# Performance work log

Hardware: AMD Instinct MI355X
Metric: run time of the kernel (lower is better)

## Reference

```python
import jax, jax.numpy as jnp
import numpy as np

MARGIN = 1.0
ALFA = 0.1


def setup_inputs() -> dict:
    key = jax.random.key(0)
    k1, k2 = jax.random.split(key)
    N, D, T = 262144, 128, 262144
    embeddings = jax.random.normal(k1, (N, D), dtype=jnp.float32)
    triplets = jax.random.randint(k2, (T, 3), 0, N, dtype=jnp.int64)
    return {"embeddings": embeddings, "triplets": triplets}


def _corr_loss(embeddings):
    # torch_cov(rowvar=False): columns are variables -> D x D covariance
    N, D = embeddings.shape
    m = embeddings - jnp.mean(embeddings, axis=0, keepdims=True)  # [N, D]
    cov = jnp.einsum('ni,nj->ij', m, m) / (N - 1)                 # [D, D]
    V = jnp.diagonal(cov)                                          # variances
    corr2 = (cov / jnp.sqrt(V[:, None] * V[None, :])) ** 2
    # strict lower triangle, n*(n-1)/2 elements, then mean
    tril = jnp.tril(jnp.ones((D, D), dtype=corr2.dtype), k=-1)
    return jnp.sum(corr2 * tril) / (D * (D - 1) / 2)


def _triplet_loss(embeddings, triplets):
    pivot = embeddings[triplets[:, 0]]
    positives = embeddings[triplets[:, 1]]
    negatives = embeddings[triplets[:, 2]]
    ap = jnp.sum((pivot - positives) ** 2, axis=1)
    an = jnp.sum((pivot - negatives) ** 2, axis=1)
    return jnp.mean(jax.nn.relu(ap - an + MARGIN))


def reference(embeddings, triplets):
    corr_loss = _corr_loss(embeddings)
    triplet_loss = _triplet_loss(embeddings, triplets)
    return triplet_loss + ALFA * corr_loss
```

## Files before the change

kernel.cpp:

```cpp
#include <hip/hip_runtime.h>

#define D 128
#define MARGIN 1.0f
#define ALFA 0.1f
#define KC 64
#define GRAMB 512
#define RBLK 520
#define TB 2048
#define GB 512

#define WS_TSUM   0
#define WS_GRAM   256
#define WS_COLSUM (WS_GRAM + D * D)
#define WS_ZERO   (WS_COLSUM + D)
#define WS_PART   16896
#define PART_STRIDE (D * D + D)
#define WS_TAB_F  (WS_PART + GRAMB * PART_STRIDE)

typedef __attribute__((ext_vector_type(8)))  short bf16x8;
typedef __attribute__((ext_vector_type(8)))  unsigned short u16x8;
typedef __attribute__((ext_vector_type(16))) float f32x16;

__device__ __forceinline__ unsigned short f2bf(float f) {
    unsigned u = __float_as_uint(f);
    u += 0x7FFFu + ((u >> 16) & 1u);
    return (unsigned short)(u >> 16);
}
__device__ __forceinline__ float bf2f(unsigned short u) {
    return __uint_as_float((unsigned)u << 16);
}

__device__ __forceinline__ void lds_barrier() {
    asm volatile("s_waitcnt lgkmcnt(0)" ::: "memory");
    __builtin_amdgcn_s_barrier();
}

__global__ __launch_bounds__(512, 4) void gram_mfma_write(const float* __restrict__ emb,
                                                          int rowsPerBlock,
                                                          float* __restrict__ ws,
                                                          unsigned short* __restrict__ tab) {
    __shared__ __align__(16) char lds[2][128 * 128];
    __shared__ float csred[D];

    const int tid = threadIdx.x;
    const int l   = tid & 63;
    const int w   = tid >> 6;
    const int r0  = blockIdx.x * rowsPerBlock;

    const int rT = w & 3;
    const int c0 = (w >> 2) * 2;

    f32x16 acc0 = {};
    f32x16 acc1 = {};
    float cs[4] = {0.f, 0.f, 0.f, 0.f};
    const int d0 = (tid & 31) * 4;

    auto stage = [&](int cc, int b) {
#pragma unroll
        for (int j = 0; j < 2; ++j) {
            const int k = j * 32 + (tid >> 5) * 2;
            const int rowg = r0 + cc * KC + k;
            const float* base = emb + (size_t)rowg * D + d0;
            float4 a  = *(const float4*)base;
            float4 bv = *(const float4*)(base + D);
            ushort4 ua, ub;
            unsigned short* pa = (unsigned short*)&ua;
            unsigned short* pb = (unsigned short*)&ub;
#pragma unroll
            for (int i = 0; i < 4; ++i) {
                float av = ((const float*)&a)[i];
                float bb = ((const float*)&bv)[i];
                cs[i] += av + bb;
                unsigned short ha = f2bf(av), hb = f2bf(bb);
                pa[i] = ha; pb[i] = hb;
                unsigned slotp = (unsigned)(k >> 3) ^ (unsigned)((tid & 31) & 7);
                unsigned off = (unsigned)(d0 + i) * 128u + slotp * 16u + (unsigned)((k & 7) << 1);
                *(unsigned*)(&lds[b][off]) = (unsigned)ha | ((unsigned)hb << 16);
            }
            *(ushort4*)&tab[(size_t)rowg * D + d0]       = ua;
            *(ushort4*)&tab[(size_t)(rowg + 1) * D + d0] = ub;
        }
    };

    auto frag = [&](int t, int kb, int b) -> bf16x8 {
        const int d = t * 32 + (l & 31);
        const int k = kb + (l >> 5) * 8;
        unsigned slotp = (unsigned)(k >> 3) ^ ((unsigned)(d >> 2) & 7u);
        return *(const bf16x8*)(&lds[b][(unsigned)d * 128u + slotp * 16u]);
    };

    const int nChunks = rowsPerBlock / KC;
    stage(0, 0);
    for (int cc = 0; cc < nChunks; ++cc) {
        const int b = cc & 1;
        lds_barrier();
        if (cc + 1 < nChunks) stage(cc + 1, b ^ 1);
#pragma unroll
        for (int kb = 0; kb < KC; kb += 16) {
            bf16x8 fr = frag(rT,     kb, b);
            bf16x8 f0 = frag(c0,     kb, b);
            bf16x8 f1 = frag(c0 + 1, kb, b);
            acc0 = __builtin_amdgcn_mfma_f32_32x32x16_bf16(fr, f0, acc0, 0, 0, 0);
            acc1 = __builtin_amdgcn_mfma_f32_32x32x16_bf16(fr, f1, acc1, 0, 0, 0);
        }
    }
    __syncthreads();

    if (tid < D) csred[tid] = 0.f;
    __syncthreads();
#pragma unroll
    for (int i = 0; i < 4; ++i) atomicAdd(&csred[d0 + i], cs[i]);
    __syncthreads();

    float* gram   = ws + WS_PART + (size_t)blockIdx.x * PART_STRIDE;
    float* colsum = gram + D * D;

    if (tid < D) colsum[tid] = csred[tid];

    const int row_hi = (l >> 5) * 4;
    const int col    = l & 31;
#pragma unroll
    for (int reg = 0; reg < 16; ++reg) {
        const int row32 = (reg & 3) + 8 * (reg >> 2) + row_hi;
        const int gr    = (rT * 32 + row32) * D;
        gram[gr + c0 * 32 + col]       = acc0[reg];
        gram[gr + (c0 + 1) * 32 + col] = acc1[reg];
    }
}

__global__ __launch_bounds__(256) void triplet_red(const unsigned short* __restrict__ tab,
                                                   const int* __restrict__ trip,
                                                   int T,
                                                   float* __restrict__ ws) {
    __shared__ float red[16];
    const int tid = threadIdx.x;

    if (blockIdx.x < RBLK) {
        const int idx   = (blockIdx.x % 65) * 256 + tid;
        const int slice = blockIdx.x / 65;
        if (idx >= PART_STRIDE) return;
        const int per = GRAMB / 8;
        const float* part = ws + WS_PART;
        float s = 0.f;
        const int p0 = slice * per;
#pragma unroll 8
        for (int p = 0; p < per; ++p)
            s += part[(size_t)(p0 + p) * PART_STRIDE + idx];
        if (idx < D * D) atomicAdd(&ws[WS_GRAM + idx], s);
        else             atomicAdd(&ws[WS_COLSUM + (idx - D * D)], s);
        return;
    }

    const int li  = tid & 15;
    const int grp = ((blockIdx.x - RBLK) * 256 + tid) >> 4;
    const int NG  = (TB * 256) >> 4;

    float wsum = 0.f;

    for (int t0 = grp; t0 < T; t0 += 6 * NG) {
        u16x8 P[6], Q[6], R[6];
#pragma unroll
        for (int u = 0; u < 6; ++u) {
            const int t = t0 + u * NG;
            if (t < T) {
                const int i0 = trip[3 * t], i1 = trip[3 * t + 1], i2 = trip[3 * t + 2];
                P[u] = *(const u16x8*)&tab[(size_t)i0 * D + li * 8];
                Q[u] = *(const u16x8*)&tab[(size_t)i1 * D + li * 8];
                R[u] = *(const u16x8*)&tab[(size_t)i2 * D + li * 8];
            }
        }
#pragma unroll
        for (int u = 0; u < 6; ++u) {
            const int t = t0 + u * NG;
            if (t < T) {
                float s = 0.f;
#pragma unroll
                for (int e = 0; e < 8; ++e) {
                    float p  = bf2f(P[u][e]);
                    float dp = p - bf2f(Q[u][e]);
                    float dn = p - bf2f(R[u][e]);
                    s += dp * dp - dn * dn;
                }
#pragma unroll
                for (int off = 8; off; off >>= 1) s += __shfl_xor(s, off, 64);
                if (li == 0) wsum += fmaxf(s + MARGIN, 0.f);
            }
        }
    }

    if (li == 0) red[tid >> 4] = wsum;
    __syncthreads();
    if (tid == 0) {
        float b = 0.f;
#pragma unroll
        for (int i = 0; i < 16; ++i) b += red[i];
        atomicAdd(&ws[WS_TSUM], b);
    }
}

__global__ __launch_bounds__(256) void finalize_kernel(const float* __restrict__ ws,
                                                       float* __restrict__ out,
                                                       int N, int T) {
    const float* gram   = ws + WS_GRAM;
    const float* colsum = ws + WS_COLSUM;

    __shared__ float V[D];
    __shared__ float red[256];

    const int tid = threadIdx.x;
    const float invN   = 1.0f / (float)N;
    const float invNm1 = 1.0f / (float)(N - 1);

    if (tid < D) {
        float m = colsum[tid] * invN;
        V[tid] = (gram[tid * D + tid] - (float)N * m * m) * invNm1;
    }
    __syncthreads();

    float local = 0.f;
    for (int idx = tid; idx < D * D; idx += 256) {
        int i = idx >> 7, j = idx & 127;
        if (j < i) {
            float mi  = colsum[i] * invN;
            float mj  = colsum[j] * invN;
            float cov = (gram[idx] - (float)N * mi * mj) * invNm1;
            local += cov * cov / (V[i] * V[j]);
        }
    }
    red[tid] = local;
    __syncthreads();
    for (int s = 128; s > 0; s >>= 1) {
        if (tid < s) red[tid] += red[tid + s];
        __syncthreads();
    }
    if (tid == 0) {
        float corr_mean = red[0] / ((float)D * (float)(D - 1) * 0.5f);
        out[0] = ws[WS_TSUM] / (float)T + ALFA * corr_mean;
    }
}

__device__ __forceinline__ float d2diff(float4 p, float4 q, float4 r) {
    float ax = p.x - q.x, ay = p.y - q.y, az = p.z - q.z, aw = p.w - q.w;
    float bx = p.x - r.x, by = p.y - r.y, bz = p.z - r.z, bw = p.w - r.w;
    return (ax * ax + ay * ay + az * az + aw * aw)
         - (bx * bx + by * by + bz * bz + bw * bw);
}

__global__ __launch_bounds__(512, 4) void fused_fallback(const float* __restrict__ emb,
                                                         const int* __restrict__ trip,
                                                         int rowsPerBlock, int T,
                                                         float* __restrict__ ws) {
    __shared__ __align__(16) char lds[2][128 * 128];
    __shared__ float csred[D];
    const int tid = threadIdx.x;

    if (blockIdx.x < GB) {
        const int l = tid & 63, w = tid >> 6, r0 = blockIdx.x * rowsPerBlock;
        const int rT = w & 3, c0 = (w >> 2) * 2;
        f32x16 acc0 = {}, acc1 = {};
        float cs[4] = {0.f, 0.f, 0.f, 0.f};
        const int d0 = (tid & 31) * 4;

        auto stage = [&](int cc, int b) {
#pragma unroll
            for (int j = 0; j < 2; ++j) {
                const int k = j * 32 + (tid >> 5) * 2;
                const float* base = emb + (size_t)(r0 + cc * 64 + k) * D + d0;
                float4 a = *(const float4*)base;
                float4 bv = *(const float4*)(base + D);
#pragma unroll
                for (int i = 0; i < 4; ++i) {
                    float av = ((const float*)&a)[i], bb = ((const float*)&bv)[i];
                    cs[i] += av + bb;
                    unsigned slotp = (unsigned)(k >> 3) ^ (unsigned)((tid & 31) & 7);
                    unsigned off = (unsigned)(d0 + i) * 128u + slotp * 16u + (unsigned)((k & 7) << 1);
                    *(unsigned*)(&lds[b][off]) = (unsigned)f2bf(av) | ((unsigned)f2bf(bb) << 16);
                }
            }
        };
        auto frag = [&](int t, int kb, int b) -> bf16x8 {
            const int d = t * 32 + (l & 31);
            const int k = kb + (l >> 5) * 8;
            unsigned slotp = (unsigned)(k >> 3) ^ ((unsigned)(d >> 2) & 7u);
            return *(const bf16x8*)(&lds[b][(unsigned)d * 128u + slotp * 16u]);
        };
        const int nChunks = rowsPerBlock / 64;
        stage(0, 0);
        for (int cc = 0; cc < nChunks; ++cc) {
            const int b = cc & 1;
            __syncthreads();
            if (cc + 1 < nChunks) stage(cc + 1, b ^ 1);
#pragma unroll
            for (int kb = 0; kb < 64; kb += 16) {
                bf16x8 fr = frag(rT, kb, b);
                bf16x8 f0 = frag(c0, kb, b);
                bf16x8 f1 = frag(c0 + 1, kb, b);
                acc0 = __builtin_amdgcn_mfma_f32_32x32x16_bf16(fr, f0, acc0, 0, 0, 0);
                acc1 = __builtin_amdgcn_mfma_f32_32x32x16_bf16(fr, f1, acc1, 0, 0, 0);
            }
        }
        __syncthreads();
        if (tid < D) csred[tid] = 0.f;
        __syncthreads();
#pragma unroll
        for (int i = 0; i < 4; ++i) atomicAdd(&csred[d0 + i], cs[i]);
        __syncthreads();
        if (tid < D) atomicAdd(&ws[WS_COLSUM + tid], csred[tid]);
        const int row_hi = (l >> 5) * 4, col = l & 31;
#pragma unroll
        for (int reg = 0; reg < 16; ++reg) {
            const int row32 = (reg & 3) + 8 * (reg >> 2) + row_hi;
            const int gr = (rT * 32 + row32) * D;
            atomicAdd(&ws[WS_GRAM + gr + c0 * 32 + col], acc0[reg]);
            atomicAdd(&ws[WS_GRAM + gr + (c0 + 1) * 32 + col], acc1[reg]);
        }
    } else {
        const int li = tid & 31, hwl = tid >> 5;
        const int hw = (blockIdx.x - GB) * 16 + hwl;
        const int NH = 1024 * 16;
        float wsum = 0.f;
        for (int t0 = hw; t0 < T; t0 += 4 * NH) {
            float4 P[4], Q[4], R[4];
#pragma unroll
            for (int k = 0; k < 4; ++k) {
                const int t = t0 + k * NH;
                if (t < T) {
                    const int i0 = trip[3 * t], i1 = trip[3 * t + 1], i2 = trip[3 * t + 2];
                    P[k] = ((const float4*)(emb + (size_t)i0 * D))[li];
                    Q[k] = ((const float4*)(emb + (size_t)i1 * D))[li];
                    R[k] = ((const float4*)(emb + (size_t)i2 * D))[li];
                }
            }
#pragma unroll
            for (int k = 0; k < 4; ++k) {
                const int t = t0 + k * NH;
                if (t < T) {
                    float s = d2diff(P[k], Q[k], R[k]);
#pragma unroll
                    for (int off = 16; off; off >>= 1) s += __shfl_xor(s, off, 64);
                    if (li == 0) wsum += fmaxf(s + MARGIN, 0.f);
                }
            }
        }
        if (li == 0) csred[hwl] = wsum;
        __syncthreads();
        if (tid == 0) {
            float b = 0.f;
#pragma unroll
            for (int i = 0; i < 16; ++i) b += csred[i];
            atomicAdd(&ws[WS_TSUM], b);
        }
    }
}

extern "C" void kernel_launch(void* const* d_in, const int* in_sizes, int n_in,
                              void* d_out, int out_size, void* d_ws, size_t ws_size,
                              hipStream_t stream) {
    const float* emb  = (const float*)d_in[0];
    const int*   trip = (const int*)d_in[1];
    float*       out  = (float*)d_out;
    float*       ws   = (float*)d_ws;

    const int N = in_sizes[0] / D;
    const int T = in_sizes[1] / 3;

    hipMemsetAsync(d_ws, 0, WS_ZERO * sizeof(float), stream);

    const size_t needB = (size_t)WS_TAB_F * 4 + (size_t)N * D * 2;

    if (ws_size >= needB) {
        unsigned short* tab = (unsigned short*)(ws + WS_TAB_F);
        gram_mfma_write<<<GRAMB, 512, 0, stream>>>(emb, N / GRAMB, ws, tab);
        triplet_red<<<RBLK + TB, 256, 0, stream>>>(tab, trip, T, ws);
    } else {
        fused_fallback<<<GB + 1024, 512, 0, stream>>>(emb, trip, N / GB, T, ws);
    }

    finalize_kernel<<<1, 256, 0, stream>>>(ws, out, N, T);
}
```

Measured before the change: 279.6 us.

## Split bf16 conversion into own kernel and co-schedule Gram MFMA with triplet gather

Separates the fp32-to-bf16 conversion and column sums into a streaming convert kernel. The Gram MFMA accumulation now reads the bf16 table and runs in the same launch as the triplet gather blocks, and the partial-Gram reduction moves to a separate kernel. The aim is to overlap the compute-bound Gram work with the latency-bound gather and to halve the partial-Gram count (256 instead of 512). The cost is an extra launch and an extra bf16 read of the table by the Gram blocks.

```diff
diff --git a/kernel.cpp b/kernel.cpp
--- a/kernel.cpp
+++ b/kernel.cpp
@@ -4,9 +4,9 @@
 #define MARGIN 1.0f
 #define ALFA 0.1f
 #define KC 64
-#define GRAMB 512
-#define RBLK 520
-#define TB 2048
+#define CVB 1024
+#define G2 256
+#define TB 1024
 #define GB 512
 
 #define WS_TSUM   0
@@ -14,8 +14,8 @@
 #define WS_COLSUM (WS_GRAM + D * D)
 #define WS_ZERO   (WS_COLSUM + D)
 #define WS_PART   16896
-#define PART_STRIDE (D * D + D)
-#define WS_TAB_F  (WS_PART + GRAMB * PART_STRIDE)
+#define PSTRIDE   (D * D)
+#define WS_TAB_F  (WS_PART + G2 * PSTRIDE)
 
 typedef __attribute__((ext_vector_type(8)))  short bf16x8;
 typedef __attribute__((ext_vector_type(8)))  unsigned short u16x8;
@@ -35,167 +35,169 @@
     __builtin_amdgcn_s_barrier();
 }
 
-__global__ __launch_bounds__(512, 4) void gram_mfma_write(const float* __restrict__ emb,
-                                                          int rowsPerBlock,
-                                                          float* __restrict__ ws,
-                                                          unsigned short* __restrict__ tab) {
-    __shared__ __align__(16) char lds[2][128 * 128];
+__global__ __launch_bounds__(512) void convert_kernel(const float* __restrict__ emb,
+                                                      int rowsPerBlock,
+                                                      float* __restrict__ ws,
+                                                      unsigned short* __restrict__ tab) {
     __shared__ float csred[D];
-
     const int tid = threadIdx.x;
-    const int l   = tid & 63;
-    const int w   = tid >> 6;
+    const int cq  = tid & 31;
+    const int rg  = tid >> 5;
     const int r0  = blockIdx.x * rowsPerBlock;
 
-    const int rT = w & 3;
-    const int c0 = (w >> 2) * 2;
-
-    f32x16 acc0 = {};
-    f32x16 acc1 = {};
-    float cs[4] = {0.f, 0.f, 0.f, 0.f};
-    const int d0 = (tid & 31) * 4;
-
-    auto stage = [&](int cc, int b) {
-#pragma unroll
-        for (int j = 0; j < 2; ++j) {
-            const int k = j * 32 + (tid >> 5) * 2;
-            const int rowg = r0 + cc * KC + k;
-            const float* base = emb + (size_t)rowg * D + d0;
-            float4 a  = *(const float4*)base;
-            float4 bv = *(const float4*)(base + D);
-            ushort4 ua, ub;
-            unsigned short* pa = (unsigned short*)&ua;
-            unsigned short* pb = (unsigned short*)&ub;
-#pragma unroll
-            for (int i = 0; i < 4; ++i) {
-                float av = ((const float*)&a)[i];
-                float bb = ((const float*)&bv)[i];
-                cs[i] += av + bb;
-                unsigned short ha = f2bf(av), hb = f2bf(bb);
-                pa[i] = ha; pb[i] = hb;
-                unsigned slotp = (unsigned)(k >> 3) ^ (unsigned)((tid & 31) & 7);
-                unsigned off = (unsigned)(d0 + i) * 128u + slotp * 16u + (unsigned)((k & 7) << 1);
-                *(unsigned*)(&lds[b][off]) = (unsigned)ha | ((unsigned)hb << 16);
-            }
-            *(ushort4*)&tab[(size_t)rowg * D + d0]       = ua;
-            *(ushort4*)&tab[(size_t)(rowg + 1) * D + d0] = ub;
-        }
-    };
-
-    auto frag = [&](int t, int kb, int b) -> bf16x8 {
-        const int d = t * 32 + (l & 31);
-        const int k = kb + (l >> 5) * 8;
-        unsigned slotp = (unsigned)(k >> 3) ^ ((unsigned)(d >> 2) & 7u);
-        return *(const bf16x8*)(&lds[b][(unsigned)d * 128u + slotp * 16u]);
-    };
-
-    const int nChunks = rowsPerBlock / KC;
-    stage(0, 0);
-    for (int cc = 0; cc < nChunks; ++cc) {
-        const int b = cc & 1;
-        lds_barrier();
-        if (cc + 1 < nChunks) stage(cc + 1, b ^ 1);
-#pragma unroll
-        for (int kb = 0; kb < KC; kb += 16) {
-            bf16x8 fr = frag(rT,     kb, b);
-            bf16x8 f0 = frag(c0,     kb, b);
-            bf16x8 f1 = frag(c0 + 1, kb, b);
-            acc0 = __builtin_amdgcn_mfma_f32_32x32x16_bf16(fr, f0, acc0, 0, 0, 0);
-            acc1 = __builtin_amdgcn_mfma_f32_32x32x16_bf16(fr, f1, acc1, 0, 0, 0);
-        }
-    }
-    __syncthreads();
+    float cs0 = 0.f, cs1 = 0.f, cs2 = 0.f, cs3 = 0.f;
+
+#pragma unroll 4
+    for (int r = rg; r < rowsPerBlock; r += 16) {
+        const float4 v = *(const float4*)(emb + (size_t)(r0 + r) * D + cq * 4);
+        cs0 += v.x; cs1 += v.y; cs2 += v.z; cs3 += v.w;
+        ushort4 u;
+        u.x = f2bf(v.x); u.y = f2bf(v.y); u.z = f2bf(v.z); u.w = f2bf(v.w);
+        *(ushort4*)&tab[(size_t)(r0 + r) * D + cq * 4] = u;
+    }
 
     if (tid < D) csred[tid] = 0.f;
     __syncthreads();
-#pragma unroll
-    for (int i = 0; i < 4; ++i) atomicAdd(&csred[d0 + i], cs[i]);
+    atomicAdd(&csred[cq * 4 + 0], cs0);
+    atomicAdd(&csred[cq * 4 + 1], cs1);
+    atomicAdd(&csred[cq * 4 + 2], cs2);
+    atomicAdd(&csred[cq * 4 + 3], cs3);
     __syncthreads();
-
-    float* gram   = ws + WS_PART + (size_t)blockIdx.x * PART_STRIDE;
-    float* colsum = gram + D * D;
-
-    if (tid < D) colsum[tid] = csred[tid];
-
-    const int row_hi = (l >> 5) * 4;
-    const int col    = l & 31;
-#pragma unroll
-    for (int reg = 0; reg < 16; ++reg) {
-        const int row32 = (reg & 3) + 8 * (reg >> 2) + row_hi;
-        const int gr    = (rT * 32 + row32) * D;
-        gram[gr + c0 * 32 + col]       = acc0[reg];
-        gram[gr + (c0 + 1) * 32 + col] = acc1[reg];
-    }
-}
-
-__global__ __launch_bounds__(256) void triplet_red(const unsigned short* __restrict__ tab,
-                                                   const int* __restrict__ trip,
-                                                   int T,
-                                                   float* __restrict__ ws) {
-    __shared__ float red[16];
+    if (tid < D) atomicAdd(&ws[WS_COLSUM + tid], csred[tid]);
+}
+
+__global__ __launch_bounds__(512, 4) void gram_trip(const unsigned short* __restrict__ tab,
+                                                    const int* __restrict__ trip,
+                                                    int T, int rowsPerBlock,
+                                                    float* __restrict__ ws) {
+    __shared__ __align__(16) char lds[2][128 * 128];
+    __shared__ float red[32];
+
     const int tid = threadIdx.x;
 
-    if (blockIdx.x < RBLK) {
-        const int idx   = (blockIdx.x % 65) * 256 + tid;
-        const int slice = blockIdx.x / 65;
-        if (idx >= PART_STRIDE) return;
-        const int per = GRAMB / 8;
-        const float* part = ws + WS_PART;
-        float s = 0.f;
-        const int p0 = slice * per;
+    if (blockIdx.x < G2) {
+        const int l  = tid & 63;
+        const int w  = tid >> 6;
+        const int r0 = blockIdx.x * rowsPerBlock;
+
+        const int rT = w & 3;
+        const int c0 = (w >> 2) * 2;
+
+        f32x16 acc0 = {};
+        f32x16 acc1 = {};
+
+        const int k0 = (tid >> 4) * 2;
+        const int dg = (tid & 15) * 8;
+
+        auto stage = [&](int cc, int b) {
+            const int rowg = r0 + cc * KC + k0;
+            u16x8 A = *(const u16x8*)&tab[(size_t)rowg * D + dg];
+            u16x8 B = *(const u16x8*)&tab[(size_t)(rowg + 1) * D + dg];
+#pragma unroll
+            for (int i = 0; i < 8; ++i) {
+                const int d = dg + i;
+                unsigned slotp = (unsigned)(k0 >> 3) ^ ((unsigned)(d >> 2) & 7u);
+                unsigned off = (unsigned)d * 128u + slotp * 16u + (unsigned)((k0 & 7) << 1);
+                *(unsigned*)(&lds[b][off]) =
+                    (unsigned)(unsigned short)A[i] | ((unsigned)(unsigned short)B[i] << 16);
+            }
+        };
+
+        auto frag = [&](int t, int kb, int b) -> bf16x8 {
+            const int d = t * 32 + (l & 31);
+            const int k = kb + (l >> 5) * 8;
+            unsigned slotp = (unsigned)(k >> 3) ^ ((unsigned)(d >> 2) & 7u);
+            return *(const bf16x8*)(&lds[b][(unsigned)d * 128u + slotp * 16u]);
+        };
+
+        const int nChunks = rowsPerBlock / KC;
+        stage(0, 0);
+        for (int cc = 0; cc < nChunks; ++cc) {
+            const int b = cc & 1;
+            lds_barrier();
+            if (cc + 1 < nChunks) stage(cc + 1, b ^ 1);
+#pragma unroll
+            for (int kb = 0; kb < KC; kb += 16) {
+                bf16x8 fr = frag(rT,     kb, b);
+                bf16x8 f0 = frag(c0,     kb, b);
+                bf16x8 f1 = frag(c0 + 1, kb, b);
+                acc0 = __builtin_amdgcn_mfma_f32_32x32x16_bf16(fr, f0, acc0, 0, 0, 0);
+                acc1 = __builtin_amdgcn_mfma_f32_32x32x16_bf16(fr, f1, acc1, 0, 0, 0);
+            }
+        }
+        __syncthreads();
+
+        float* gram = ws + WS_PART + (size_t)blockIdx.x * PSTRIDE;
+
+        const int row_hi = (l >> 5) * 4;
+        const int col    = l & 31;
+#pragma unroll
+        for (int reg = 0; reg < 16; ++reg) {
+            const int row32 = (reg & 3) + 8 * (reg >> 2) + row_hi;
+            const int gr    = (rT * 32 + row32) * D;
+            gram[gr + c0 * 32 + col]       = acc0[reg];
+            gram[gr + (c0 + 1) * 32 + col] = acc1[reg];
+        }
+    } else {
+        const int li  = tid & 15;
+        const int grp = (blockIdx.x - G2) * 32 + (tid >> 4);
+        const int NG  = TB * 32;
+
+        float wsum = 0.f;
+
+        for (int t0 = grp; t0 < T; t0 += 4 * NG) {
+            u16x8 P[4], Q[4], R[4];
+#pragma unroll
+            for (int u = 0; u < 4; ++u) {
+                const int t = t0 + u * NG;
+                if (t < T) {
+                    const int i0 = trip[3 * t], i1 = trip[3 * t + 1], i2 = trip[3 * t + 2];
+                    P[u] = *(const u16x8*)&tab[(size_t)i0 * D + li * 8];
+                    Q[u] = *(const u16x8*)&tab[(size_t)i1 * D + li * 8];
+                    R[u] = *(const u16x8*)&tab[(size_t)i2 * D + li * 8];
+                }
+            }
+#pragma unroll
+            for (int u = 0; u < 4; ++u) {
+                const int t = t0 + u * NG;
+                if (t < T) {
+                    float s = 0.f;
+#pragma unroll
+                    for (int e = 0; e < 8; ++e) {
+                        float p  = bf2f(P[u][e]);
+                        float dp = p - bf2f(Q[u][e]);
+                        float dn = p - bf2f(R[u][e]);
+                        s += dp * dp - dn * dn;
+                    }
+#pragma unroll
+                    for (int off = 8; off; off >>= 1) s += __shfl_xor(s, off, 64);
+                    if (li == 0) wsum += fmaxf(s + MARGIN, 0.f);
+                }
+            }
+        }
+
+        if (li == 0) red[tid >> 4] = wsum;
+        __syncthreads();
+        if (tid == 0) {
+            float b = 0.f;
+#pragma unroll
+            for (int i = 0; i < 32; ++i) b += red[i];
+            atomicAdd(&ws[WS_TSUM], b);
+        }
+    }
+}
+
+__global__ __launch_bounds__(512) void reduce_partials(float* __restrict__ ws) {
+    const int idx   = (blockIdx.x & 31) * 512 + threadIdx.x;
+    const int slice = blockIdx.x >> 5;
+    const int per   = G2 / 8;
+    const float* part = ws + WS_PART;
+    float s = 0.f;
+    const int p0 = slice * per;
 #pragma unroll 8
-        for (int p = 0; p < per; ++p)
-            s += part[(size_t)(p0 + p) * PART_STRIDE + idx];
-        if (idx < D * D) atomicAdd(&ws[WS_GRAM + idx], s);
-        else             atomicAdd(&ws[WS_COLSUM + (idx - D * D)], s);
-        return;
-    }
-
-    const int li  = tid & 15;
-    const int grp = ((blockIdx.x - RBLK) * 256 + tid) >> 4;
-    const int NG  = (TB * 256) >> 4;
-
-    float wsum = 0.f;
-
-    for (int t0 = grp; t0 < T; t0 += 6 * NG) {
-        u16x8 P[6], Q[6], R[6];
-#pragma unroll
-        for (int u = 0; u < 6; ++u) {
-            const int t = t0 + u * NG;
-            if (t < T) {
-                const int i0 = trip[3 * t], i1 = trip[3 * t + 1], i2 = trip[3 * t + 2];
-                P[u] = *(const u16x8*)&tab[(size_t)i0 * D + li * 8];
-                Q[u] = *(const u16x8*)&tab[(size_t)i1 * D + li * 8];
-                R[u] = *(const u16x8*)&tab[(size_t)i2 * D + li * 8];
-            }
-        }
-#pragma unroll
-        for (int u = 0; u < 6; ++u) {
-            const int t = t0 + u * NG;
-            if (t < T) {
-                float s = 0.f;
-#pragma unroll
-                for (int e = 0; e < 8; ++e) {
-                    float p  = bf2f(P[u][e]);
-                    float dp = p - bf2f(Q[u][e]);
-                    float dn = p - bf2f(R[u][e]);
-                    s += dp * dp - dn * dn;
-                }
-#pragma unroll
-                for (int off = 8; off; off >>= 1) s += __shfl_xor(s, off, 64);
-                if (li == 0) wsum += fmaxf(s + MARGIN, 0.f);
-            }
-        }
-    }
-
-    if (li == 0) red[tid >> 4] = wsum;
-    __syncthreads();
-    if (tid == 0) {
-        float b = 0.f;
-#pragma unroll
-        for (int i = 0; i < 16; ++i) b += red[i];
-        atomicAdd(&ws[WS_TSUM], b);
-    }
+    for (int p = 0; p < per; ++p)
+        s += part[(size_t)(p0 + p) * PSTRIDE + idx];
+    atomicAdd(&ws[WS_GRAM + idx], s);
 }
 
 __global__ __launch_bounds__(256) void finalize_kernel(const float* __restrict__ ws,
@@ -370,8 +372,9 @@
 
     if (ws_size >= needB) {
         unsigned short* tab = (unsigned short*)(ws + WS_TAB_F);
-        gram_mfma_write<<<GRAMB, 512, 0, stream>>>(emb, N / GRAMB, ws, tab);
-        triplet_red<<<RBLK + TB, 256, 0, stream>>>(tab, trip, T, ws);
+        convert_kernel<<<CVB, 512, 0, stream>>>(emb, N / CVB, ws, tab);
+        gram_trip<<<G2 + TB, 512, 0, stream>>>(tab, trip, T, N / G2, ws);
+        reduce_partials<<<256, 512, 0, stream>>>(ws);
     } else {
         fused_fallback<<<GB + 1024, 512, 0, stream>>>(emb, trip, N / GB, T, ws);
     }
```

Result: faster. 272.8 us (-2.4%).
